# Optimization experiments

Measured on AMD Instinct MI355X. Metric: run time of the kernel, lower is better.

Reference implementation:

```python
import jax, jax.numpy as jnp
import numpy as np

NUM_HEADS = 8
LN_EPS = 1e-5


def setup_inputs() -> dict:
    key = jax.random.key(0)
    ks = jax.random.split(key, 8)
    B, H, W, C = 2, 64, 64, 256
    return {
        "x": jax.random.normal(ks[0], (B, H, W, C), dtype=jnp.float32),
        "cond": jax.random.normal(ks[1], (B, C), dtype=jnp.float32),
        "t": jax.random.randint(ks[2], (B,), 0, 100, dtype=jnp.int64),
        "emb_table": jax.random.normal(ks[3], (100, C), dtype=jnp.float32) * 0.02,
        "ada_w": jax.random.normal(ks[4], (C, 2 * C), dtype=jnp.float32) * 0.02,
        "ada_b": jnp.zeros((2 * C,), dtype=jnp.float32),
        "qkv_w": jax.random.normal(ks[5], (C, 3 * C), dtype=jnp.float32) * 0.02,
        "qkv_b": jnp.zeros((3 * C,), dtype=jnp.float32),
        "proj_w": jax.random.normal(ks[6], (C, C), dtype=jnp.float32) * 0.02,
        "proj_b": jnp.zeros((C,), dtype=jnp.float32),
    }


def reference(x, cond, t, emb_table, ada_w, ada_b, qkv_w, qkv_b, proj_w, proj_b):
    B, H, W, C = x.shape
    N = H * W
    h = NUM_HEADS
    d = C // h
    scale = d ** -0.5

    x = x.reshape(B, N, C)

    # AdaLayerNorm (adalayernorm_abs): timestep embedding -> SiLU -> Linear -> scale/shift
    emb = emb_table[t]                                # [B, C]
    ss = jax.nn.silu(emb) @ ada_w + ada_b             # [B, 2C]
    sc, sh = jnp.split(ss, 2, axis=-1)                # each [B, C]
    mu = jnp.mean(x, axis=-1, keepdims=True)
    var = jnp.var(x, axis=-1, keepdims=True)
    xn = (x - mu) * jax.lax.rsqrt(var + LN_EPS)       # LN without affine
    x = xn * (1.0 + sc[:, None, :]) + sh[:, None, :]

    # QKV projection and head split
    qkv = (x @ qkv_w + qkv_b).reshape(B, N, 3, h, d)
    qkv = jnp.transpose(qkv, (2, 0, 3, 1, 4))          # [3, B, h, N, d]
    q, k, v = qkv[0], qkv[1], qkv[2]

    # Manual attention: full [B, h, N, N] scores (matches original module)
    attn = jnp.einsum('bhnd,bhmd->bhnm', q, k) * scale
    attn = jax.nn.softmax(attn, axis=-1)
    out = jnp.einsum('bhnm,bhmd->bhnd', attn, v)       # [B, h, N, d]
    out = jnp.transpose(out, (0, 2, 1, 3)).reshape(B, N, C)

    out = (out.reshape(B, H, W, C) @ proj_w) + proj_b
    return out
```

## Files before the change

### kernel.cpp

```cpp
#include <hip/hip_runtime.h>
#include <hip/hip_bf16.h>
#include <stdint.h>

typedef __attribute__((ext_vector_type(8))) short bfrag;
typedef __attribute__((ext_vector_type(4))) short bfrag4;
typedef __attribute__((ext_vector_type(4))) float f32x4;
typedef __attribute__((ext_vector_type(2))) float f32x2;
typedef __attribute__((ext_vector_type(2))) unsigned int u32x2;
typedef __attribute__((ext_vector_type(4))) unsigned int u32x4;

__device__ inline short f2bf(float f) {
  union { float f; uint32_t u; } v; v.f = f;
  uint32_t u = v.u;
  uint32_t r = (u + 0x7fffu + ((u >> 16) & 1u)) >> 16;
  return (short)r;
}
__device__ inline float bf2f(short s) {
  return __builtin_bit_cast(float, (uint32_t)((uint32_t)(uint16_t)s << 16));
}

#if __has_builtin(__builtin_amdgcn_cvt_pk_bf16_f32)
typedef __attribute__((ext_vector_type(2))) __bf16 bf16x2_t;
__device__ inline uint32_t pack_bf16(float a, float b) {
  bf16x2_t r = __builtin_amdgcn_cvt_pk_bf16_f32(a, b);
  return __builtin_bit_cast(uint32_t, r);
}
#else
__device__ inline uint32_t pack_bf16(float a, float b) {
  uint32_t ua = __builtin_bit_cast(uint32_t, a) + 0x8000u;
  uint32_t ub = __builtin_bit_cast(uint32_t, b) + 0x8000u;
  return __builtin_amdgcn_perm(ub, ua, 0x07060302);
}
#endif

__device__ inline void lds_barrier() {
  asm volatile("s_waitcnt lgkmcnt(0)" ::: "memory");
  __builtin_amdgcn_s_barrier();
  asm volatile("" ::: "memory");
}

__global__ __launch_bounds__(256) void prep_kernel(
    const float* __restrict__ emb_table, const int* __restrict__ t,
    const float* __restrict__ ada_w, const float* __restrict__ ada_b,
    float* __restrict__ scsh,
    const float* __restrict__ qkv_w, short* __restrict__ qkv_wt,
    const float* __restrict__ proj_w, short* __restrict__ proj_wt) {
  __shared__ float smem[64 * 65];
  const int blk = blockIdx.x;
  const int tid = threadIdx.x;
  if (blk < 16) {
    float* se = smem;
    float* part = smem + 256;
    int b = blk >> 3, ox = blk & 7;
    int tt = t[b];
    float e = emb_table[tt * 256 + tid];
    se[tid] = e / (1.f + __expf(-e));
    __syncthreads();
    int ol = tid & 63, kc = tid >> 6;
    int o = ox * 64 + ol;
    float acc = 0.f;
#pragma unroll 8
    for (int k = kc * 64; k < (kc + 1) * 64; ++k) acc += se[k] * ada_w[k * 512 + o];
    part[tid] = acc;
    __syncthreads();
    if (tid < 64) {
      int oo = ox * 64 + tid;
      scsh[b * 512 + oo] =
          part[tid] + part[64 + tid] + part[128 + tid] + part[192 + tid] + ada_b[oo];
    }
  } else {
    const float* W; short* Wt; int N, lb;
    if (blk < 64) { W = qkv_w; Wt = qkv_wt; N = 768; lb = blk - 16; }
    else          { W = proj_w; Wt = proj_wt; N = 256; lb = blk - 64; }
    float (*tile)[65] = (float(*)[65])smem;
    int k0 = (lb & 3) * 64, n0 = (lb >> 2) * 64;
    int r = tid >> 2, c0 = (tid & 3) * 16;
    const float* src = W + (long)(k0 + r) * N + n0 + c0;
#pragma unroll
    for (int j = 0; j < 16; j += 4) {
      float4 v = *(const float4*)(src + j);
      tile[r][c0 + j] = v.x; tile[r][c0 + j + 1] = v.y;
      tile[r][c0 + j + 2] = v.z; tile[r][c0 + j + 3] = v.w;
    }
    __syncthreads();
    int nl = tid >> 2, kc = (tid & 3) * 16;
    short outv[16];
#pragma unroll
    for (int j = 0; j < 16; ++j) outv[j] = f2bf(tile[kc + j][nl]);
    short* dst = Wt + (long)(n0 + nl) * 256 + k0 + kc;
    *(bfrag*)dst = *(bfrag*)&outv[0];
    *(bfrag*)(dst + 8) = *(bfrag*)&outv[8];
  }
}

__global__ __launch_bounds__(256) void ln_kernel(const float* __restrict__ x,
                                                 const float* __restrict__ scsh,
                                                 short* __restrict__ xb) {
  int row = blockIdx.x * 4 + (threadIdx.x >> 6);
  int b = row >> 12;
  int lane = threadIdx.x & 63;
  float4 v = *(const float4*)(x + (long)row * 256 + lane * 4);
  float s = v.x + v.y + v.z + v.w;
  float sq = v.x * v.x + v.y * v.y + v.z * v.z + v.w * v.w;
#pragma unroll
  for (int off = 32; off > 0; off >>= 1) {
    s += __shfl_xor(s, off);
    sq += __shfl_xor(sq, off);
  }
  float mu = s * (1.f / 256.f);
  float var = sq * (1.f / 256.f) - mu * mu;
  float rstd = rsqrtf(var + 1e-5f);
  const float* scp = scsh + b * 512 + lane * 4;
  float4 sc = *(const float4*)scp;
  float4 sh = *(const float4*)(scp + 256);
  float y0 = (v.x - mu) * rstd * (1.f + sc.x) + sh.x;
  float y1 = (v.y - mu) * rstd * (1.f + sc.y) + sh.y;
  float y2 = (v.z - mu) * rstd * (1.f + sc.z) + sh.z;
  float y3 = (v.w - mu) * rstd * (1.f + sc.w) + sh.w;
  u32x2 o; o.x = pack_bf16(y0, y1); o.y = pack_bf16(y2, y3);
  *(u32x2*)&xb[(long)row * 256 + lane * 4] = o;
}

__global__ __launch_bounds__(256) void gemm_qkv(const short* __restrict__ A,
                                                const short* __restrict__ Bt,
                                                const float* __restrict__ bias,
                                                float qscale,
                                                short* __restrict__ qk,
                                                short* __restrict__ vT) {
  __shared__ short As[128 * 40];
  __shared__ short Bs[64 * 40];
  const int mt = blockIdx.x, nt = blockIdx.y;
  const int tid = threadIdx.x;
  const int w = tid >> 6, lane = tid & 63, l16 = lane & 15, quad = lane >> 4;
  const int ar = tid >> 1, ak = (tid & 1) * 16;
  const int br = tid >> 2, bk = (tid & 3) * 8;
  f32x4 acc[2][4] = {};
  const short* Arow = A + (long)(mt * 128 + ar) * 256 + ak;
  const short* Brow = Bt + (long)(nt * 64 + br) * 256 + bk;
  bfrag a8a = *(const bfrag*)Arow;
  bfrag a8b = *(const bfrag*)(Arow + 8);
  bfrag b8  = *(const bfrag*)Brow;
  for (int kk = 0; kk < 8; ++kk) {
    __syncthreads();
    *(bfrag*)&As[ar * 40 + ak] = a8a;
    *(bfrag*)&As[ar * 40 + ak + 8] = a8b;
    *(bfrag*)&Bs[br * 40 + bk] = b8;
    __syncthreads();
    int kn = (kk < 7) ? (kk + 1) : 7;
    a8a = *(const bfrag*)(Arow + kn * 32);
    a8b = *(const bfrag*)(Arow + kn * 32 + 8);
    b8  = *(const bfrag*)(Brow + kn * 32);
    bfrag a0 = *(const bfrag*)&As[(w * 32 + l16) * 40 + quad * 8];
    bfrag a1 = *(const bfrag*)&As[(w * 32 + 16 + l16) * 40 + quad * 8];
#pragma unroll
    for (int c = 0; c < 4; ++c) {
      bfrag bf = *(const bfrag*)&Bs[(c * 16 + l16) * 40 + quad * 8];
      acc[0][c] = __builtin_amdgcn_mfma_f32_16x16x32_bf16(a0, bf, acc[0][c], 0, 0, 0);
      acc[1][c] = __builtin_amdgcn_mfma_f32_16x16x32_bf16(a1, bf, acc[1][c], 0, 0, 0);
    }
  }
  const int rowb = mt * 128 + w * 32 + quad * 4;
  if (nt < 8) {
#pragma unroll
    for (int rg = 0; rg < 2; ++rg) {
      int row0 = rowb + rg * 16;
#pragma unroll
      for (int c = 0; c < 4; ++c) {
        int col = nt * 64 + c * 16 + l16;
        float bv = bias[col];
        float mult = (col < 256) ? qscale : 1.0f;
#pragma unroll
        for (int r = 0; r < 4; ++r)
          qk[(long)(row0 + r) * 512 + col] = f2bf((acc[rg][c][r] + bv) * mult);
      }
    }
  } else {
    const int bb = mt >> 5;
#pragma unroll
    for (int rg = 0; rg < 2; ++rg) {
      int keyl = (rowb + rg * 16) & 4095;
#pragma unroll
      for (int c = 0; c < 4; ++c) {
        int col = nt * 64 + c * 16 + l16;
        float bv = bias[col];
        int d = col - 512;
        u32x2 dd;
        dd.x = pack_bf16(acc[rg][c][0] + bv, acc[rg][c][1] + bv);
        dd.y = pack_bf16(acc[rg][c][2] + bv, acc[rg][c][3] + bv);
        *(u32x2*)&vT[((long)(bb * 8 + (d >> 5)) * 32 + (d & 31)) * 4096 + keyl] = dd;
      }
    }
  }
}

__global__ __launch_bounds__(256) void attn_kernel(const short* __restrict__ qk,
                                                   const short* __restrict__ vT,
                                                   short* __restrict__ OpB,
                                                   float* __restrict__ lpart) {
  const int bid = blockIdx.x;
  const int c = bid & 7, j = bid >> 3;
  const int bh = c * 2 + (j >> 7);
  const int qt = j & 31;
  const int ks = (j >> 5) & 3;
  const int b = bh >> 3, hh = bh & 7;
  const int tid = threadIdx.x;
  const int w = tid >> 6, lane = tid & 63, l16 = lane & 15, quad = lane >> 4;
  const int sig0 = ((l16 >> 2) * 8) + (l16 & 3);

  __shared__ short Ks[2][128 * 36];
  __shared__ short Vt[2][32 * 132];

  const long rowbase = (long)b * 4096;
  const int qrow0 = qt * 128 + w * 32 + l16;
  bfrag qf[2];
#pragma unroll
  for (int g = 0; g < 2; ++g)
    qf[g] = *(const bfrag*)&qk[(rowbase + qrow0 + g * 16) * 512 + hh * 32 + quad * 8];

  f32x4 olo[2] = {}, ohi[2] = {};
  f32x2 lsum[2] = {};

  const int si = tid >> 2, sk = (tid & 3) * 8;
  const int vrow = tid >> 3, vcol = (tid & 7) * 8;
  const short* ksrc = qk + rowbase * 512 + 256 + hh * 32 + (long)si * 512 + sk;
  const short* vsrc = vT + ((long)bh * 32 + vrow) * 4096 + vcol;

  const int kbase = ks * 1024;
  bfrag k8a = *(const bfrag*)(ksrc + (long)kbase * 512);
  bfrag k8b = *(const bfrag*)(ksrc + (long)(kbase + 64) * 512);
  bfrag v8a = *(const bfrag*)(vsrc + kbase);
  bfrag v8b = *(const bfrag*)(vsrc + kbase + 64);

  int buf = 0;
  for (int i = 0; i < 8; ++i) {
    *(bfrag*)&Ks[buf][si * 36 + sk] = k8a;
    *(bfrag*)&Ks[buf][(si + 64) * 36 + sk] = k8b;
    *(bfrag*)&Vt[buf][vrow * 132 + vcol] = v8a;
    *(bfrag*)&Vt[buf][vrow * 132 + 64 + vcol] = v8b;
    lds_barrier();
    int nn = (i < 7) ? (i + 1) : 7;
    int kb_n = kbase + nn * 128;
    k8a = *(const bfrag*)(ksrc + (long)kb_n * 512);
    k8b = *(const bfrag*)(ksrc + (long)(kb_n + 64) * 512);
    v8a = *(const bfrag*)(vsrc + kb_n);
    v8b = *(const bfrag*)(vsrc + kb_n + 64);

#pragma unroll
    for (int p = 0; p < 4; ++p) {
      const int kb = p * 32;
      bfrag kf0 = *(const bfrag*)&Ks[buf][(kb + sig0) * 36 + quad * 8];
      bfrag kf1 = *(const bfrag*)&Ks[buf][(kb + sig0 + 4) * 36 + quad * 8];
      f32x4 z = {0, 0, 0, 0};
      f32x4 s0[2], s1[2];
      __builtin_amdgcn_s_setprio(1);
      s0[0] = __builtin_amdgcn_mfma_f32_16x16x32_bf16(kf0, qf[0], z, 0, 0, 0);
      s0[1] = __builtin_amdgcn_mfma_f32_16x16x32_bf16(kf0, qf[1], z, 0, 0, 0);
      s1[0] = __builtin_amdgcn_mfma_f32_16x16x32_bf16(kf1, qf[0], z, 0, 0, 0);
      s1[1] = __builtin_amdgcn_mfma_f32_16x16x32_bf16(kf1, qf[1], z, 0, 0, 0);
      __builtin_amdgcn_s_setprio(0);
      bfrag pb[2];
#pragma unroll
      for (int g = 0; g < 2; ++g) {
        float e0 = __builtin_amdgcn_exp2f(s0[g][0]);
        float e1 = __builtin_amdgcn_exp2f(s0[g][1]);
        float e2 = __builtin_amdgcn_exp2f(s0[g][2]);
        float e3 = __builtin_amdgcn_exp2f(s0[g][3]);
        float f0 = __builtin_amdgcn_exp2f(s1[g][0]);
        float f1 = __builtin_amdgcn_exp2f(s1[g][1]);
        float f2 = __builtin_amdgcn_exp2f(s1[g][2]);
        float f3 = __builtin_amdgcn_exp2f(s1[g][3]);
        f32x2 pa = {e0, e1}, pbv = {e2, e3}, pc = {f0, f1}, pd = {f2, f3};
        lsum[g] += pa; lsum[g] += pbv; lsum[g] += pc; lsum[g] += pd;
        u32x4 pk;
        pk.x = pack_bf16(e0, e1); pk.y = pack_bf16(e2, e3);
        pk.z = pack_bf16(f0, f1); pk.w = pack_bf16(f2, f3);
        pb[g] = __builtin_bit_cast(bfrag, pk);
      }
      bfrag vlo = *(const bfrag*)&Vt[buf][l16 * 132 + kb + quad * 8];
      bfrag vhi = *(const bfrag*)&Vt[buf][(16 + l16) * 132 + kb + quad * 8];
      __builtin_amdgcn_s_setprio(1);
#pragma unroll
      for (int g = 0; g < 2; ++g) {
        olo[g] = __builtin_amdgcn_mfma_f32_16x16x32_bf16(pb[g], vlo, olo[g], 0, 0, 0);
        ohi[g] = __builtin_amdgcn_mfma_f32_16x16x32_bf16(pb[g], vhi, ohi[g], 0, 0, 0);
      }
      __builtin_amdgcn_s_setprio(0);
    }
    buf ^= 1;
  }
  uint16_t* Ob = (uint16_t*)OpB;
  const long obase = ((long)ks * 16 + bh) * 4096;
  const int qgb = qt * 128 + w * 32;
#pragma unroll
  for (int g = 0; g < 2; ++g) {
    float ls = lsum[g].x + lsum[g].y;
    ls += __shfl_xor(ls, 16); ls += __shfl_xor(ls, 32);
    if (quad == 0)
      lpart[obase + qrow0 + g * 16] = ls;
#pragma unroll
    for (int r = 0; r < 4; ++r) {
      int q = qgb + g * 16 + quad * 4 + r;
      uint32_t pk = pack_bf16(olo[g][r], ohi[g][r]);
      Ob[(obase + q) * 32 + l16] = (uint16_t)pk;
      Ob[(obase + q) * 32 + l16 + 16] = (uint16_t)(pk >> 16);
    }
  }
}

__global__ __launch_bounds__(256) void proj_kernel(const short* __restrict__ OpB,
                                                   const float* __restrict__ lpart,
                                                   const short* __restrict__ Bt,
                                                   const float* __restrict__ bias,
                                                   float* __restrict__ out) {
  __shared__ short As[128 * 40];
  __shared__ short Bs[64 * 40];
  const int mt = blockIdx.x, nt = blockIdx.y;
  const int tid = threadIdx.x;
  const int w = tid >> 6, lane = tid & 63, l16 = lane & 15, quad = lane >> 4;
  const int ar = tid >> 1, ak = (tid & 1) * 16;
  const int br = tid >> 2, bk = (tid & 3) * 8;
  f32x4 acc[2][4] = {};

  const int row = mt * 128 + ar;
  const int q = row & 4095, bq = row >> 12;
  const short* Brow = Bt + (long)(nt * 64 + br) * 256 + bk;

  long lb0 = (long)(bq * 8) * 4096 + q;
  bfrag pa[4][2];
  f32x4 pl;
#pragma unroll
  for (int ks = 0; ks < 4; ++ks) {
    long base = (lb0 + (long)ks * 16 * 4096) * 32 + ak;
    pa[ks][0] = *(const bfrag*)&OpB[base];
    pa[ks][1] = *(const bfrag*)&OpB[base + 8];
    pl[ks] = lpart[lb0 + (long)ks * 16 * 4096];
  }
  bfrag b8 = *(const bfrag*)Brow;

  for (int kk = 0; kk < 8; ++kk) {
    float linv = 1.f / (pl[0] + pl[1] + pl[2] + pl[3]);
    short av[16];
#pragma unroll
    for (int h = 0; h < 2; ++h) {
#pragma unroll
      for (int j = 0; j < 8; j += 2) {
        float v0 = (bf2f(pa[0][h][j]) + bf2f(pa[1][h][j]) +
                    bf2f(pa[2][h][j]) + bf2f(pa[3][h][j])) * linv;
        float v1 = (bf2f(pa[0][h][j+1]) + bf2f(pa[1][h][j+1]) +
                    bf2f(pa[2][h][j+1]) + bf2f(pa[3][h][j+1])) * linv;
        *(uint32_t*)&av[h * 8 + j] = pack_bf16(v0, v1);
      }
    }
    __syncthreads();
    *(bfrag*)&As[ar * 40 + ak] = *(bfrag*)&av[0];
    *(bfrag*)&As[ar * 40 + ak + 8] = *(bfrag*)&av[8];
    *(bfrag*)&Bs[br * 40 + bk] = b8;
    __syncthreads();
    int kn = (kk < 7) ? (kk + 1) : 7;
    long lbn = (long)(bq * 8 + kn) * 4096 + q;
#pragma unroll
    for (int ks = 0; ks < 4; ++ks) {
      long base = (lbn + (long)ks * 16 * 4096) * 32 + ak;
      pa[ks][0] = *(const bfrag*)&OpB[base];
      pa[ks][1] = *(const bfrag*)&OpB[base + 8];
      pl[ks] = lpart[lbn + (long)ks * 16 * 4096];
    }
    b8 = *(const bfrag*)(Brow + kn * 32);

    bfrag a0 = *(const bfrag*)&As[(w * 32 + l16) * 40 + quad * 8];
    bfrag a1 = *(const bfrag*)&As[(w * 32 + 16 + l16) * 40 + quad * 8];
#pragma unroll
    for (int c = 0; c < 4; ++c) {
      bfrag bf = *(const bfrag*)&Bs[(c * 16 + l16) * 40 + quad * 8];
      acc[0][c] = __builtin_amdgcn_mfma_f32_16x16x32_bf16(a0, bf, acc[0][c], 0, 0, 0);
      acc[1][c] = __builtin_amdgcn_mfma_f32_16x16x32_bf16(a1, bf, acc[1][c], 0, 0, 0);
    }
  }
  const int rowb = mt * 128 + w * 32 + quad * 4;
#pragma unroll
  for (int rg = 0; rg < 2; ++rg) {
    int row0 = rowb + rg * 16;
#pragma unroll
    for (int c = 0; c < 4; ++c) {
      int col = nt * 64 + c * 16 + l16;
      float bv = bias[col];
#pragma unroll
      for (int r = 0; r < 4; ++r)
        out[(long)(row0 + r) * 256 + col] = acc[rg][c][r] + bv;
    }
  }
}

extern "C" void kernel_launch(void* const* d_in, const int* in_sizes, int n_in,
                              void* d_out, int out_size, void* d_ws, size_t ws_size,
                              hipStream_t stream) {
  const float* x      = (const float*)d_in[0];
  const int*   t      = (const int*)d_in[2];
  const float* emb    = (const float*)d_in[3];
  const float* ada_w  = (const float*)d_in[4];
  const float* ada_b  = (const float*)d_in[5];
  const float* qkv_w  = (const float*)d_in[6];
  const float* qkv_b  = (const float*)d_in[7];
  const float* proj_w = (const float*)d_in[8];
  const float* proj_b = (const float*)d_in[9];

  char* ws = (char*)d_ws;
  float* scsh     = (float*)(ws);
  short* qkv_wt   = (short*)(ws + 4096);
  short* proj_wt  = (short*)(ws + 397312);
  short* xb       = (short*)(ws + 528384);
  short* qk_out   = (short*)(ws + 4722688);
  short* vT       = (short*)(ws + 13111296);
  short* OpB      = (short*)(ws + 21499904);
  float* lpart    = (float*)(ws + 38277120);

  const float QS = 0.17677669529663687f * 1.4426950408889634f;

  prep_kernel<<<80, 256, 0, stream>>>(emb, t, ada_w, ada_b, scsh,
                                      qkv_w, qkv_wt, proj_w, proj_wt);
  ln_kernel<<<2048, 256, 0, stream>>>(x, scsh, xb);
  gemm_qkv<<<dim3(64, 12), 256, 0, stream>>>(xb, qkv_wt, qkv_b, QS, qk_out, vT);
  attn_kernel<<<2048, 256, 0, stream>>>(qk_out, vT, OpB, lpart);
  proj_kernel<<<dim3(64, 4), 256, 0, stream>>>(OpB, lpart, proj_wt, proj_b,
                                               (float*)d_out);
}
```

Baseline: 164.2 us.

## Compute softmax row sums via MFMA with ones vector and unroll key blocks by two

Replaces the VALU accumulation of exponentials for the softmax denominator with an extra MFMA against an all-ones bf16 operand, so the row sums come out of the matrix unit directly. The sums now use bf16-rounded probabilities, matching the values fed to the PV product. The inner loop also processes two 32-key sub-blocks per iteration, hoisting K and V fragment loads to give more independent MFMAs for scheduling. This adds a third of extra PV MFMA work and more register pressure, in exchange for removing the per-element float adds and the cross-lane shuffles at the end.

```diff
diff --git a/kernel.cpp b/kernel.cpp
--- a/kernel.cpp
+++ b/kernel.cpp
@@ -217,8 +217,10 @@
   for (int g = 0; g < 2; ++g)
     qf[g] = *(const bfrag*)&qk[(rowbase + qrow0 + g * 16) * 512 + hh * 32 + quad * 8];
 
-  f32x4 olo[2] = {}, ohi[2] = {};
-  f32x2 lsum[2] = {};
+  f32x4 olo[2] = {}, ohi[2] = {}, osum[2] = {};
+  bfrag vones;
+#pragma unroll
+  for (int jj = 0; jj < 8; ++jj) vones[jj] = (short)0x3F80;
 
   const int si = tid >> 2, sk = (tid & 3) * 8;
   const int vrow = tid >> 3, vcol = (tid & 7) * 8;
@@ -246,43 +248,63 @@
     v8b = *(const bfrag*)(vsrc + kb_n + 64);
 
 #pragma unroll
-    for (int p = 0; p < 4; ++p) {
-      const int kb = p * 32;
-      bfrag kf0 = *(const bfrag*)&Ks[buf][(kb + sig0) * 36 + quad * 8];
-      bfrag kf1 = *(const bfrag*)&Ks[buf][(kb + sig0 + 4) * 36 + quad * 8];
+    for (int h = 0; h < 2; ++h) {
+      const int kb0 = h * 64, kb1 = h * 64 + 32;
+      bfrag kA0 = *(const bfrag*)&Ks[buf][(kb0 + sig0) * 36 + quad * 8];
+      bfrag kA1 = *(const bfrag*)&Ks[buf][(kb0 + sig0 + 4) * 36 + quad * 8];
+      bfrag kB0 = *(const bfrag*)&Ks[buf][(kb1 + sig0) * 36 + quad * 8];
+      bfrag kB1 = *(const bfrag*)&Ks[buf][(kb1 + sig0 + 4) * 36 + quad * 8];
+      bfrag vAlo = *(const bfrag*)&Vt[buf][l16 * 132 + kb0 + quad * 8];
+      bfrag vAhi = *(const bfrag*)&Vt[buf][(16 + l16) * 132 + kb0 + quad * 8];
+      bfrag vBlo = *(const bfrag*)&Vt[buf][l16 * 132 + kb1 + quad * 8];
+      bfrag vBhi = *(const bfrag*)&Vt[buf][(16 + l16) * 132 + kb1 + quad * 8];
       f32x4 z = {0, 0, 0, 0};
-      f32x4 s0[2], s1[2];
+      f32x4 sA0[2], sA1[2], sB0[2], sB1[2];
       __builtin_amdgcn_s_setprio(1);
-      s0[0] = __builtin_amdgcn_mfma_f32_16x16x32_bf16(kf0, qf[0], z, 0, 0, 0);
-      s0[1] = __builtin_amdgcn_mfma_f32_16x16x32_bf16(kf0, qf[1], z, 0, 0, 0);
-      s1[0] = __builtin_amdgcn_mfma_f32_16x16x32_bf16(kf1, qf[0], z, 0, 0, 0);
-      s1[1] = __builtin_amdgcn_mfma_f32_16x16x32_bf16(kf1, qf[1], z, 0, 0, 0);
+#pragma unroll
+      for (int g = 0; g < 2; ++g) {
+        sA0[g] = __builtin_amdgcn_mfma_f32_16x16x32_bf16(kA0, qf[g], z, 0, 0, 0);
+        sA1[g] = __builtin_amdgcn_mfma_f32_16x16x32_bf16(kA1, qf[g], z, 0, 0, 0);
+        sB0[g] = __builtin_amdgcn_mfma_f32_16x16x32_bf16(kB0, qf[g], z, 0, 0, 0);
+        sB1[g] = __builtin_amdgcn_mfma_f32_16x16x32_bf16(kB1, qf[g], z, 0, 0, 0);
+      }
       __builtin_amdgcn_s_setprio(0);
-      bfrag pb[2];
+      bfrag pbA[2], pbB[2];
 #pragma unroll
       for (int g = 0; g < 2; ++g) {
-        float e0 = __builtin_amdgcn_exp2f(s0[g][0]);
-        float e1 = __builtin_amdgcn_exp2f(s0[g][1]);
-        float e2 = __builtin_amdgcn_exp2f(s0[g][2]);
-        float e3 = __builtin_amdgcn_exp2f(s0[g][3]);
-        float f0 = __builtin_amdgcn_exp2f(s1[g][0]);
-        float f1 = __builtin_amdgcn_exp2f(s1[g][1]);
-        float f2 = __builtin_amdgcn_exp2f(s1[g][2]);
-        float f3 = __builtin_amdgcn_exp2f(s1[g][3]);
-        f32x2 pa = {e0, e1}, pbv = {e2, e3}, pc = {f0, f1}, pd = {f2, f3};
-        lsum[g] += pa; lsum[g] += pbv; lsum[g] += pc; lsum[g] += pd;
-        u32x4 pk;
-        pk.x = pack_bf16(e0, e1); pk.y = pack_bf16(e2, e3);
-        pk.z = pack_bf16(f0, f1); pk.w = pack_bf16(f2, f3);
-        pb[g] = __builtin_bit_cast(bfrag, pk);
-      }
-      bfrag vlo = *(const bfrag*)&Vt[buf][l16 * 132 + kb + quad * 8];
-      bfrag vhi = *(const bfrag*)&Vt[buf][(16 + l16) * 132 + kb + quad * 8];
+        float a0 = __builtin_amdgcn_exp2f(sA0[g][0]);
+        float a1 = __builtin_amdgcn_exp2f(sA0[g][1]);
+        float a2 = __builtin_amdgcn_exp2f(sA0[g][2]);
+        float a3 = __builtin_amdgcn_exp2f(sA0[g][3]);
+        float a4 = __builtin_amdgcn_exp2f(sA1[g][0]);
+        float a5 = __builtin_amdgcn_exp2f(sA1[g][1]);
+        float a6 = __builtin_amdgcn_exp2f(sA1[g][2]);
+        float a7 = __builtin_amdgcn_exp2f(sA1[g][3]);
+        float b0 = __builtin_amdgcn_exp2f(sB0[g][0]);
+        float b1 = __builtin_amdgcn_exp2f(sB0[g][1]);
+        float b2 = __builtin_amdgcn_exp2f(sB0[g][2]);
+        float b3 = __builtin_amdgcn_exp2f(sB0[g][3]);
+        float b4 = __builtin_amdgcn_exp2f(sB1[g][0]);
+        float b5 = __builtin_amdgcn_exp2f(sB1[g][1]);
+        float b6 = __builtin_amdgcn_exp2f(sB1[g][2]);
+        float b7 = __builtin_amdgcn_exp2f(sB1[g][3]);
+        u32x4 pka, pkb;
+        pka.x = pack_bf16(a0, a1); pka.y = pack_bf16(a2, a3);
+        pka.z = pack_bf16(a4, a5); pka.w = pack_bf16(a6, a7);
+        pkb.x = pack_bf16(b0, b1); pkb.y = pack_bf16(b2, b3);
+        pkb.z = pack_bf16(b4, b5); pkb.w = pack_bf16(b6, b7);
+        pbA[g] = __builtin_bit_cast(bfrag, pka);
+        pbB[g] = __builtin_bit_cast(bfrag, pkb);
+      }
       __builtin_amdgcn_s_setprio(1);
 #pragma unroll
       for (int g = 0; g < 2; ++g) {
-        olo[g] = __builtin_amdgcn_mfma_f32_16x16x32_bf16(pb[g], vlo, olo[g], 0, 0, 0);
-        ohi[g] = __builtin_amdgcn_mfma_f32_16x16x32_bf16(pb[g], vhi, ohi[g], 0, 0, 0);
+        olo[g]  = __builtin_amdgcn_mfma_f32_16x16x32_bf16(pbA[g], vAlo, olo[g], 0, 0, 0);
+        ohi[g]  = __builtin_amdgcn_mfma_f32_16x16x32_bf16(pbA[g], vAhi, ohi[g], 0, 0, 0);
+        osum[g] = __builtin_amdgcn_mfma_f32_16x16x32_bf16(pbA[g], vones, osum[g], 0, 0, 0);
+        olo[g]  = __builtin_amdgcn_mfma_f32_16x16x32_bf16(pbB[g], vBlo, olo[g], 0, 0, 0);
+        ohi[g]  = __builtin_amdgcn_mfma_f32_16x16x32_bf16(pbB[g], vBhi, ohi[g], 0, 0, 0);
+        osum[g] = __builtin_amdgcn_mfma_f32_16x16x32_bf16(pbB[g], vones, osum[g], 0, 0, 0);
       }
       __builtin_amdgcn_s_setprio(0);
     }
@@ -293,10 +315,8 @@
   const int qgb = qt * 128 + w * 32;
 #pragma unroll
   for (int g = 0; g < 2; ++g) {
-    float ls = lsum[g].x + lsum[g].y;
-    ls += __shfl_xor(ls, 16); ls += __shfl_xor(ls, 32);
-    if (quad == 0)
-      lpart[obase + qrow0 + g * 16] = ls;
+    if (l16 == 0)
+      *(f32x4*)&lpart[obase + qgb + g * 16 + quad * 4] = osum[g];
 #pragma unroll
     for (int r = 0; r < 4; ++r) {
       int q = qgb + g * 16 + quad * 4 + r;
```

Result: no change. 163.2 us, median of 3 (-0.6%).
